# Performance work log

Hardware: AMD Instinct MI355X
Metric: run time of the kernel (lower is better)

## Reference

```python
import jax, jax.numpy as jnp
import numpy as np

B = 1024      # batch of seed nodes
S = 16        # sample_size
H = 256       # hidden
IN = 150      # in_dim + NUM_CLASS (128 + 22)
OUT = 22
HEADS = 8
NN = 100000   # number of graph nodes
LN_EPS = 1e-5


def setup_inputs() -> dict:
    key = jax.random.key(0)
    ks = jax.random.split(key, 16)
    sc = 0.05
    return {
        "node_feats": jax.random.normal(ks[0], (NN, IN), jnp.float32),
        "batch": jax.random.randint(ks[1], (B,), 0, NN),
        "nbr2": jax.random.randint(ks[2], (B, S), 0, NN),
        "nbr1": jax.random.randint(ks[3], (B * (S + 1), S), 0, NN),
        "W_in": jax.random.normal(ks[4], (IN, H), jnp.float32) * sc,
        "b_in": jnp.zeros((H,), jnp.float32),
        "Wqkv": jax.random.normal(ks[5], (2, 3, H, H), jnp.float32) * sc,
        "bqkv": jnp.zeros((2, 3, H), jnp.float32),
        "Wo": jax.random.normal(ks[6], (2, H, H), jnp.float32) * sc,
        "bo": jnp.zeros((2, H), jnp.float32),
        "Wf": jax.random.normal(ks[7], (2, H, H), jnp.float32) * sc,
        "bf": jnp.zeros((2, H), jnp.float32),
        "ln_g": jnp.ones((4, H), jnp.float32),
        "ln_b": jnp.zeros((4, H), jnp.float32),
        "W_out": jax.random.normal(ks[8], (H, OUT), jnp.float32) * sc,
        "b_out": jnp.zeros((OUT,), jnp.float32),
    }


def _layer_norm(x, g, b):
    m = jnp.mean(x, axis=-1, keepdims=True)
    v = jnp.mean((x - m) ** 2, axis=-1, keepdims=True)
    return (x - m) * jax.lax.rsqrt(v + LN_EPS) * g + b


def _mha(q, kv, Wq, Wk, Wv, bq, bk, bv, Wout, bout):
    # q: [N, 1, H], kv: [N, S, H]; single-query multi-head attention
    N, Sk, _ = kv.shape
    dh = H // HEADS
    qp = (q @ Wq + bq).reshape(N, 1, HEADS, dh)
    kp = (kv @ Wk + bk).reshape(N, Sk, HEADS, dh)
    vp = (kv @ Wv + bv).reshape(N, Sk, HEADS, dh)
    att = jax.nn.softmax(
        jnp.einsum("nqhd,nkhd->nhqk", qp, kp) / np.float32(np.sqrt(dh)), axis=-1
    )
    o = jnp.einsum("nhqk,nkhd->nqhd", att, vp).reshape(N, 1, H)
    return o @ Wout + bout


def _attn_block(x, l, Wqkv, bqkv, Wo, bo, Wf, bf, ln_g, ln_b):
    # x: [N, S+1, H]; slot 0 is the query (self), rest are sampled neighbors
    q, kv = x[:, 0:1, :], x[:, 1:, :]
    h = _mha(q, kv, Wqkv[l, 0], Wqkv[l, 1], Wqkv[l, 2],
             bqkv[l, 0], bqkv[l, 1], bqkv[l, 2], Wo[l], bo[l])
    h = h[:, 0, :] + q[:, 0, :]                       # residual
    h = _layer_norm(h, ln_g[2 * l], ln_b[2 * l])
    h = h + (h @ Wf[l] + bf[l])                       # FFN (single Linear) + residual
    return _layer_norm(h, ln_g[2 * l + 1], ln_b[2 * l + 1])


def reference(node_feats, batch, nbr2, nbr1, W_in, b_in, Wqkv, bqkv, Wo, bo,
              Wf, bf, ln_g, ln_b, W_out, b_out):
    # Recursive neighbor expansion (unrolled for layers=2)
    ids1 = jnp.concatenate([batch[:, None], nbr2], axis=1).reshape(-1)   # [B*(S+1)]
    ids0 = jnp.concatenate([ids1[:, None], nbr1], axis=1).reshape(-1)    # [B*(S+1)^2]
    # layer 0: proj_in(features) = ReLU(Linear) (Dropout identity in eval)
    h0 = jax.nn.relu(node_feats[ids0] @ W_in + b_in)                     # [M0, H]
    # layer 1
    h1 = _attn_block(h0.reshape(B * (S + 1), S + 1, H), 0,
                     Wqkv, bqkv, Wo, bo, Wf, bf, ln_g, ln_b)
    # layer 2
    h2 = _attn_block(h1.reshape(B, S + 1, H), 1,
                     Wqkv, bqkv, Wo, bo, Wf, bf, ln_g, ln_b)
    # proj_out: Linear -> Softmax
    return jax.nn.softmax(h2 @ W_out + b_out, axis=-1)
```

## Files before the change

### kernel.cpp

```cpp
#include <hip/hip_runtime.h>
#include <hip/hip_bf16.h>
#include <math.h>

typedef unsigned short ushort_t;
typedef __bf16 bf16x8 __attribute__((ext_vector_type(8)));
typedef float  f32x4  __attribute__((ext_vector_type(4)));

#define B_SZ   1024
#define SEQ    17
#define KVN    16
#define HDIM   256
#define NHEAD  8
#define DH     32
#define INF    150
#define OUTD   22
#define LN_EPS 1e-5f
#define N1     (B_SZ * SEQ)
#define NN_    100000
#define NKVBLK 1563
#define NHQBLK 272

constexpr size_t SZ_H0    = (size_t)NN_ * 256 * 2;
constexpr size_t SZ_KV0   = (size_t)NN_ * 512 * 2;
constexpr size_t SZ_ROW   = (size_t)N1 * 256 * 2;
constexpr size_t OFF_HQ   = 0;
constexpr size_t OFF_KV0  = OFF_HQ + SZ_H0;
constexpr size_t OFF_QKV1 = OFF_KV0;
constexpr size_t OFF_O1   = OFF_QKV1 + (size_t)N1 * 768 * 2;
constexpr size_t OFF_H2   = OFF_O1 + (size_t)B_SZ * 256 * 2;
constexpr size_t OFF_Q0   = OFF_KV0 + SZ_KV0;
constexpr size_t OFF_O0   = OFF_Q0 + SZ_ROW;
constexpr size_t OFF_H1   = OFF_O0;
constexpr size_t OFF_IDS  = OFF_O0 + SZ_ROW;
constexpr size_t OFF_WTIN = OFF_IDS + (size_t)N1 * 4;
constexpr size_t OFF_WKV0 = OFF_WTIN + 256 * 160 * 2;
constexpr size_t OFF_WQ0  = OFF_WKV0 + 512 * 256 * 2;
constexpr size_t OFF_WKVQ1= OFF_WQ0 + 256 * 256 * 2;
constexpr size_t OFF_WO0  = OFF_WKVQ1 + 768 * 256 * 2;
constexpr size_t OFF_WF0  = OFF_WO0 + 256 * 256 * 2;
constexpr size_t OFF_WO1  = OFF_WF0 + 256 * 256 * 2;
constexpr size_t OFF_WF1  = OFF_WO1 + 256 * 256 * 2;
constexpr size_t OFF_B1   = OFF_WF1 + 256 * 256 * 2;

__device__ __forceinline__ ushort_t f2bfu(float x) {
    __hip_bfloat16 h = __float2bfloat16(x);
    return *reinterpret_cast<ushort_t*>(&h);
}
__device__ __forceinline__ float bfu2f(ushort_t u) {
    __hip_bfloat16 h;
    *reinterpret_cast<ushort_t*>(&h) = u;
    return __bfloat162float(h);
}
__device__ __forceinline__ f32x4 mfma16(bf16x8 a, bf16x8 b, f32x4 c) {
    return __builtin_amdgcn_mfma_f32_16x16x32_bf16(a, b, c, 0, 0, 0);
}

__global__ __launch_bounds__(256) void k_prep(
    const float* __restrict__ W_in, const float* __restrict__ Wqkv,
    const float* __restrict__ Wo, const float* __restrict__ Wf,
    const float* __restrict__ bqkv,
    const int* __restrict__ batch, const int* __restrict__ nbr2,
    char* __restrict__ ws) {
    const int job = blockIdx.y;
    const int idx = blockIdx.x * 256 + threadIdx.x;
    if (job == 11) {
        if (idx < N1) {
            int b = idx / SEQ, s = idx % SEQ;
            ((int*)(ws + OFF_IDS))[idx] = (s == 0) ? batch[b] : nbr2[b * KVN + s - 1];
        }
        return;
    }
    if (job == 12) {
        if (idx < 768) ((float*)(ws + OFF_B1))[idx] = bqkv[768 + ((idx + 256) % 768)];
        return;
    }
    const float* src = nullptr; ushort_t* dst = nullptr;
    int Kpad = 256, Kvalid = 256;
    switch (job) {
        case 0:  src = W_in;           dst = (ushort_t*)(ws + OFF_WTIN); Kpad = 160; Kvalid = 150; break;
        case 1:  src = Wqkv + 65536;   dst = (ushort_t*)(ws + OFF_WKV0); break;
        case 2:  src = Wqkv + 131072;  dst = (ushort_t*)(ws + OFF_WKV0) + 65536; break;
        case 3:  src = Wqkv;           dst = (ushort_t*)(ws + OFF_WQ0); break;
        case 4:  src = Wqkv + 262144;  dst = (ushort_t*)(ws + OFF_WKVQ1); break;
        case 5:  src = Wqkv + 327680;  dst = (ushort_t*)(ws + OFF_WKVQ1) + 65536; break;
        case 6:  src = Wqkv + 196608;  dst = (ushort_t*)(ws + OFF_WKVQ1) + 131072; break;
        case 7:  src = Wo;             dst = (ushort_t*)(ws + OFF_WO0); break;
        case 8:  src = Wo + 65536;     dst = (ushort_t*)(ws + OFF_WO1); break;
        case 9:  src = Wf;             dst = (ushort_t*)(ws + OFF_WF0); break;
        case 10: src = Wf + 65536;     dst = (ushort_t*)(ws + OFF_WF1); break;
    }
    const int total = 256 * Kpad;
    if (idx >= total) return;
    int n = idx / Kpad, k = idx % Kpad;
    dst[idx] = (k < Kvalid) ? f2bfu(src[(size_t)k * 256 + n]) : (ushort_t)0;
}

__global__ __launch_bounds__(256) void k_fused(
    const float* __restrict__ nf,
    const ushort_t* __restrict__ Wt_in, const float* __restrict__ b_in,
    const ushort_t* __restrict__ Wkv, const ushort_t* __restrict__ Wq,
    const float* __restrict__ bqkv, const int* __restrict__ ids1,
    ushort_t* __restrict__ kv0, ushort_t* __restrict__ hq,
    ushort_t* __restrict__ q0) {
    __shared__ ushort_t Ah[64 * 256];
    __shared__ ushort_t Sh[4][32][72];
    const int tid = threadIdx.x;
    const bool iskv = blockIdx.x < NKVBLK;
    const int m0 = (iskv ? blockIdx.x : blockIdx.x - NKVBLK) * 64;
    const int lane = tid & 63, w = tid >> 6;
    const int lr = lane & 15, q4 = lane >> 4, lk = q4 * 8;

    {
        ushort_t (*Astage)[168] = reinterpret_cast<ushort_t (*)[168]>(Ah);
        #pragma unroll
        for (int i = 0; i < 5; ++i) {
            int flat = tid + i * 256;
            int row = flat / 20, ch = flat % 20;
            int gm; bool valid;
            if (iskv) { gm = m0 + row; valid = gm < NN_; if (!valid) gm = 0; }
            else      { gm = ids1[m0 + row]; valid = true; }
            const float* ap = nf + (size_t)gm * INF + ch * 8;
            ushort_t tmp[8];
            if (valid && ch < 18) {
                #pragma unroll
                for (int j = 0; j < 4; ++j) {
                    float2 f = *reinterpret_cast<const float2*>(ap + j * 2);
                    tmp[j * 2] = f2bfu(f.x); tmp[j * 2 + 1] = f2bfu(f.y);
                }
            } else {
                #pragma unroll
                for (int j = 0; j < 8; ++j) {
                    int k = ch * 8 + j;
                    tmp[j] = (valid && k < INF) ? f2bfu(ap[j]) : (ushort_t)0;
                }
            }
            *reinterpret_cast<int4*>(&Astage[row][ch * 8]) = *reinterpret_cast<int4*>(tmp);
        }
    }
    __syncthreads();

    f32x4 acc[4][4] = {};
    {
        ushort_t (*Astage)[168] = reinterpret_cast<ushort_t (*)[168]>(Ah);
        bf16x8 bc[4];
        #pragma unroll
        for (int ni = 0; ni < 4; ++ni)
            bc[ni] = *reinterpret_cast<const bf16x8*>(
                Wt_in + (size_t)(w * 64 + ni * 16 + lr) * 160 + lk);
        #pragma unroll
        for (int s = 0; s < 5; ++s) {
            bf16x8 bn[4];
            if (s < 4) {
                #pragma unroll
                for (int ni = 0; ni < 4; ++ni)
                    bn[ni] = *reinterpret_cast<const bf16x8*>(
                        Wt_in + (size_t)(w * 64 + ni * 16 + lr) * 160 + (s + 1) * 32 + lk);
            }
            bf16x8 a[4];
            #pragma unroll
            for (int mi = 0; mi < 4; ++mi)
                a[mi] = *reinterpret_cast<const bf16x8*>(&Astage[mi * 16 + lr][s * 32 + lk]);
            #pragma unroll
            for (int mi = 0; mi < 4; ++mi)
                #pragma unroll
                for (int ni = 0; ni < 4; ++ni)
                    acc[mi][ni] = mfma16(a[mi], bc[ni], acc[mi][ni]);
            if (s < 4) {
                #pragma unroll
                for (int ni = 0; ni < 4; ++ni) bc[ni] = bn[ni];
            }
        }
    }
    __syncthreads();

    #pragma unroll
    for (int ni = 0; ni < 4; ++ni) {
        int col = w * 64 + ni * 16 + lr;
        float bb = b_in[col];
        #pragma unroll
        for (int mi = 0; mi < 4; ++mi)
            #pragma unroll
            for (int r = 0; r < 4; ++r) {
                int row = mi * 16 + q4 * 4 + r;
                Ah[row * 256 + (col ^ ((row & 7) << 3))] =
                    f2bfu(fmaxf(acc[mi][ni][r] + bb, 0.f));
            }
    }
    __syncthreads();

    if (!iskv) {
        #pragma unroll
        for (int i = 0; i < 8; ++i) {
            int flat = tid + i * 256;
            int row = flat >> 5, ch = flat & 31;
            *reinterpret_cast<int4*>(hq + (size_t)(m0 + row) * 256 + ch * 8) =
                *reinterpret_cast<const int4*>(&Ah[row * 256 + (ch ^ (row & 7)) * 8]);
        }
    }

    const int nh = iskv ? 2 : 1;
    for (int h = 0; h < nh; ++h) {
        const ushort_t* Bm = iskv ? (Wkv + (size_t)h * 256 * 256) : Wq;
        const float* bias = iskv ? (bqkv + 256 + h * 256) : bqkv;
        f32x4 acc2[4][4] = {};
        bf16x8 bc[4];
        #pragma unroll
        for (int ni = 0; ni < 4; ++ni)
            bc[ni] = *reinterpret_cast<const bf16x8*>(
                Bm + (size_t)(w * 64 + ni * 16 + lr) * 256 + lk);
        #pragma unroll
        for (int s = 0; s < 8; ++s) {
            bf16x8 bn[4];
            if (s < 7) {
                #pragma unroll
                for (int ni = 0; ni < 4; ++ni)
                    bn[ni] = *reinterpret_cast<const bf16x8*>(
                        Bm + (size_t)(w * 64 + ni * 16 + lr) * 256 + (s + 1) * 32 + lk);
            }
            bf16x8 a[4];
            #pragma unroll
            for (int mi = 0; mi < 4; ++mi) {
                int row = mi * 16 + lr;
                int chunk = (s * 4 + q4) ^ (row & 7);
                a[mi] = *reinterpret_cast<const bf16x8*>(&Ah[row * 256 + chunk * 8]);
            }
            #pragma unroll
            for (int mi = 0; mi < 4; ++mi)
                #pragma unroll
                for (int ni = 0; ni < 4; ++ni)
                    acc2[mi][ni] = mfma16(a[mi], bc[ni], acc2[mi][ni]);
            if (s < 7) {
                #pragma unroll
                for (int ni = 0; ni < 4; ++ni) bc[ni] = bn[ni];
            }
        }
        float bl[4];
        #pragma unroll
        for (int ni = 0; ni < 4; ++ni) bl[ni] = bias[w * 64 + ni * 16 + lr];
        ushort_t* outp = iskv ? kv0 : q0;
        const int ldo = iskv ? 512 : 256;
        const int coff = (iskv ? h * 256 : 0) + w * 64;
        #pragma unroll
        for (int part = 0; part < 2; ++part) {
            #pragma unroll
            for (int mi2 = 0; mi2 < 2; ++mi2) {
                int mi = part * 2 + mi2;
                #pragma unroll
                for (int ni = 0; ni < 4; ++ni)
                    #pragma unroll
                    for (int r = 0; r < 4; ++r)
                        Sh[w][mi2 * 16 + q4 * 4 + r][ni * 16 + lr] =
                            f2bfu(acc2[mi][ni][r] + bl[ni]);
            }
            #pragma unroll
            for (int j = 0; j < 4; ++j) {
                int flat = lane + j * 64;
                int r32 = flat >> 3, ch = flat & 7;
                int grow = m0 + part * 32 + r32;
                if (!iskv || grow < NN_)
                    *reinterpret_cast<int4*>(outp + (size_t)grow * ldo + coff + ch * 8) =
                        *reinterpret_cast<const int4*>(&Sh[w][r32][ch * 8]);
            }
        }
    }
}

__global__ __launch_bounds__(256) void k_ffn(
    const ushort_t* __restrict__ Ain, const ushort_t* __restrict__ W1t,
    const float* __restrict__ b1,
    const ushort_t* __restrict__ resmat, int rstride,
    const float* __restrict__ lng1, const float* __restrict__ lnb1,
    const ushort_t* __restrict__ W2t, const float* __restrict__ b2,
    const float* __restrict__ lng2, const float* __restrict__ lnb2,
    ushort_t* __restrict__ out) {
    __shared__ ushort_t Al[32][264];
    __shared__ float xr[32][260];
    __shared__ float mrow[32], rrow[32];
    const int tid = threadIdx.x;
    const int m0 = blockIdx.x * 32;
    const int lane = tid & 63, w = tid >> 6;
    const int lr = lane & 15, q4 = lane >> 4, lk = q4 * 8;

    #pragma unroll
    for (int j = 0; j < 4; ++j) {
        int flat = tid + j * 256;
        int row = flat >> 5, ch = flat & 31;
        *reinterpret_cast<int4*>(&Al[row][ch * 8]) =
            *reinterpret_cast<const int4*>(Ain + (size_t)(m0 + row) * 256 + ch * 8);
    }
    __syncthreads();

    f32x4 acc[2][4];
    #pragma unroll
    for (int g = 0; g < 2; ++g) {
        const ushort_t* Wt = g ? W2t : W1t;
        #pragma unroll
        for (int mi = 0; mi < 2; ++mi)
            #pragma unroll
            for (int ni = 0; ni < 4; ++ni) acc[mi][ni] = f32x4{0.f, 0.f, 0.f, 0.f};
        bf16x8 bc[4];
        #pragma unroll
        for (int ni = 0; ni < 4; ++ni)
            bc[ni] = *reinterpret_cast<const bf16x8*>(
                Wt + (size_t)(w * 64 + ni * 16 + lr) * 256 + lk);
        #pragma unroll
        for (int s = 0; s < 8; ++s) {
            bf16x8 bn[4];
            if (s < 7) {
                #pragma unroll
                for (int ni = 0; ni < 4; ++ni)
                    bn[ni] = *reinterpret_cast<const bf16x8*>(
                        Wt + (size_t)(w * 64 + ni * 16 + lr) * 256 + (s + 1) * 32 + lk);
            }
            bf16x8 a0 = *reinterpret_cast<const bf16x8*>(&Al[lr][s * 32 + lk]);
            bf16x8 a1 = *reinterpret_cast<const bf16x8*>(&Al[16 + lr][s * 32 + lk]);
            #pragma unroll
            for (int ni = 0; ni < 4; ++ni) {
                acc[0][ni] = mfma16(a0, bc[ni], acc[0][ni]);
                acc[1][ni] = mfma16(a1, bc[ni], acc[1][ni]);
            }
            if (s < 7) {
                #pragma unroll
                for (int ni = 0; ni < 4; ++ni) bc[ni] = bn[ni];
            }
        }
        #pragma unroll
        for (int mi = 0; mi < 2; ++mi)
            #pragma unroll
            for (int ni = 0; ni < 4; ++ni)
                #pragma unroll
                for (int r = 0; r < 4; ++r)
                    xr[mi * 16 + q4 * 4 + r][w * 64 + ni * 16 + lr] = acc[mi][ni][r];
        __syncthreads();
        {
            float bb = g ? b2[tid] : b1[tid];
            if (g == 0) {
                for (int r = 0; r < 32; ++r)
                    xr[r][tid] += bb + bfu2f(resmat[(size_t)(m0 + r) * rstride * 256 + tid]);
            } else {
                for (int r = 0; r < 32; ++r)
                    xr[r][tid] += bb + bfu2f(Al[r][tid]);
            }
        }
        __syncthreads();
        for (int rr = w * 8; rr < w * 8 + 8; ++rr) {
            float4 v = *reinterpret_cast<const float4*>(&xr[rr][lane * 4]);
            float s1 = v.x + v.y + v.z + v.w;
            float s2 = v.x * v.x + v.y * v.y + v.z * v.z + v.w * v.w;
            #pragma unroll
            for (int off = 32; off > 0; off >>= 1) {
                s1 += __shfl_xor(s1, off);
                s2 += __shfl_xor(s2, off);
            }
            if (lane == 0) {
                float m = s1 * (1.f / 256.f);
                float var = s2 * (1.f / 256.f) - m * m;
                mrow[rr] = m;
                rrow[rr] = rsqrtf(var + LN_EPS);
            }
        }
        __syncthreads();
        if (g == 0) {
            float gg = lng1[tid], bb = lnb1[tid];
            for (int r = 0; r < 32; ++r)
                Al[r][tid] = f2bfu((xr[r][tid] - mrow[r]) * rrow[r] * gg + bb);
        } else {
            float gg = lng2[tid], bb = lnb2[tid];
            for (int r = 0; r < 32; ++r)
                out[(size_t)(m0 + r) * 256 + tid] =
                    f2bfu((xr[r][tid] - mrow[r]) * rrow[r] * gg + bb);
        }
        __syncthreads();
    }
}

__global__ __launch_bounds__(256) void k_qkv1(
    const ushort_t* __restrict__ h1, const ushort_t* __restrict__ Wt,
    const float* __restrict__ bias, ushort_t* __restrict__ outm) {
    __shared__ ushort_t Ah[64 * 256];
    __shared__ ushort_t Sh[4][32][72];
    const int tid = threadIdx.x;
    const int m0 = blockIdx.x * 64;
    const int lane = tid & 63, w = tid >> 6;
    const int lr = lane & 15, q4 = lane >> 4, lk = q4 * 8;

    #pragma unroll
    for (int i = 0; i < 8; ++i) {
        int flat = tid + i * 256;
        int row = flat >> 5, ch = flat & 31;
        *reinterpret_cast<int4*>(&Ah[row * 256 + ((ch ^ (row & 7)) * 8)]) =
            *reinterpret_cast<const int4*>(h1 + (size_t)(m0 + row) * 256 + ch * 8);
    }
    __syncthreads();

    for (int p = 0; p < 3; ++p) {
        f32x4 acc[4][4] = {};
        bf16x8 bc[4];
        #pragma unroll
        for (int ni = 0; ni < 4; ++ni)
            bc[ni] = *reinterpret_cast<const bf16x8*>(
                Wt + (size_t)(p * 256 + w * 64 + ni * 16 + lr) * 256 + lk);
        #pragma unroll
        for (int s = 0; s < 8; ++s) {
            bf16x8 bn[4];
            if (s < 7) {
                #pragma unroll
                for (int ni = 0; ni < 4; ++ni)
                    bn[ni] = *reinterpret_cast<const bf16x8*>(
                        Wt + (size_t)(p * 256 + w * 64 + ni * 16 + lr) * 256 + (s + 1) * 32 + lk);
            }
            bf16x8 a[4];
            #pragma unroll
            for (int mi = 0; mi < 4; ++mi) {
                int row = mi * 16 + lr;
                int chunk = (s * 4 + q4) ^ (row & 7);
                a[mi] = *reinterpret_cast<const bf16x8*>(&Ah[row * 256 + chunk * 8]);
            }
            #pragma unroll
            for (int mi = 0; mi < 4; ++mi)
                #pragma unroll
                for (int ni = 0; ni < 4; ++ni)
                    acc[mi][ni] = mfma16(a[mi], bc[ni], acc[mi][ni]);
            if (s < 7) {
                #pragma unroll
                for (int ni = 0; ni < 4; ++ni) bc[ni] = bn[ni];
            }
        }
        float bl[4];
        #pragma unroll
        for (int ni = 0; ni < 4; ++ni) bl[ni] = bias[p * 256 + w * 64 + ni * 16 + lr];
        const int coff = p * 256 + w * 64;
        #pragma unroll
        for (int part = 0; part < 2; ++part) {
            #pragma unroll
            for (int mi2 = 0; mi2 < 2; ++mi2) {
                int mi = part * 2 + mi2;
                #pragma unroll
                for (int ni = 0; ni < 4; ++ni)
                    #pragma unroll
                    for (int r = 0; r < 4; ++r)
                        Sh[w][mi2 * 16 + q4 * 4 + r][ni * 16 + lr] =
                            f2bfu(acc[mi][ni][r] + bl[ni]);
            }
            #pragma unroll
            for (int j = 0; j < 4; ++j) {
                int flat = lane + j * 64;
                int r32 = flat >> 3, ch = flat & 7;
                int grow = m0 + part * 32 + r32;
                *reinterpret_cast<int4*>(outm + (size_t)grow * 768 + coff + ch * 8) =
                    *reinterpret_cast<const int4*>(&Sh[w][r32][ch * 8]);
            }
        }
    }
}

__global__ __launch_bounds__(256) void attn_wave(
    const ushort_t* __restrict__ q_all, int qld, int qoff, int qstride,
    const ushort_t* __restrict__ kv_all, int kvld, int koff, int voff,
    const int* __restrict__ kvidx, int ngroups, ushort_t* __restrict__ o_out) {
    __shared__ ushort_t KL[4][KVN][264];
    __shared__ ushort_t VL[4][KVN][264];
    const int w = threadIdx.x >> 6, lane = threadIdx.x & 63;
    const int g = blockIdx.x * 4 + w;
    if (g >= ngroups) return;

    int idx16 = 0;
    if (lane < KVN)
        idx16 = kvidx ? kvidx[g * KVN + lane] : g * SEQ + 1 + lane;

    float qv[4];
    {
        uint2 u = *reinterpret_cast<const uint2*>(
            q_all + (size_t)g * qstride * qld + qoff + lane * 4);
        qv[0] = bfu2f((ushort_t)(u.x & 0xffff));
        qv[1] = bfu2f((ushort_t)(u.x >> 16));
        qv[2] = bfu2f((ushort_t)(u.y & 0xffff));
        qv[3] = bfu2f((ushort_t)(u.y >> 16));
    }
    {
        const int r = lane & 15, qtr = lane >> 4;
        int rid = __shfl(idx16, r);
        const ushort_t* kb = kv_all + (size_t)rid * kvld + koff;
        const ushort_t* vb = kv_all + (size_t)rid * kvld + voff;
        #pragma unroll
        for (int j = 0; j < 8; ++j) {
            int c8 = (qtr * 8 + j) * 8;
            *reinterpret_cast<int4*>(&KL[w][r][c8]) = *reinterpret_cast<const int4*>(kb + c8);
            *reinterpret_cast<int4*>(&VL[w][r][c8]) = *reinterpret_cast<const int4*>(vb + c8);
        }
    }
    float att[KVN];
    #pragma unroll
    for (int k = 0; k < KVN; ++k) {
        uint2 u = *reinterpret_cast<const uint2*>(&KL[w][k][lane * 4]);
        float p = qv[0] * bfu2f((ushort_t)(u.x & 0xffff))
                + qv[1] * bfu2f((ushort_t)(u.x >> 16))
                + qv[2] * bfu2f((ushort_t)(u.y & 0xffff))
                + qv[3] * bfu2f((ushort_t)(u.y >> 16));
        p += __shfl_xor(p, 1);
        p += __shfl_xor(p, 2);
        p += __shfl_xor(p, 4);
        att[k] = p * 0.17677669529663687f;
    }
    float m = att[0];
    #pragma unroll
    for (int k = 1; k < KVN; ++k) m = fmaxf(m, att[k]);
    float sum = 0.f;
    #pragma unroll
    for (int k = 0; k < KVN; ++k) { att[k] = __expf(att[k] - m); sum += att[k]; }
    float inv = 1.f / sum;
    float o[4] = {0.f, 0.f, 0.f, 0.f};
    #pragma unroll
    for (int k = 0; k < KVN; ++k) {
        uint2 u = *reinterpret_cast<const uint2*>(&VL[w][k][lane * 4]);
        float a = att[k] * inv;
        o[0] += a * bfu2f((ushort_t)(u.x & 0xffff));
        o[1] += a * bfu2f((ushort_t)(u.x >> 16));
        o[2] += a * bfu2f((ushort_t)(u.y & 0xffff));
        o[3] += a * bfu2f((ushort_t)(u.y >> 16));
    }
    uint2 r;
    r.x = (unsigned)f2bfu(o[0]) | ((unsigned)f2bfu(o[1]) << 16);
    r.y = (unsigned)f2bfu(o[2]) | ((unsigned)f2bfu(o[3]) << 16);
    *reinterpret_cast<uint2*>(o_out + (size_t)g * 256 + lane * 4) = r;
}

__global__ __launch_bounds__(64) void k_out(
    const ushort_t* __restrict__ h2, const float* __restrict__ W_out,
    const float* __restrict__ b_out, float* __restrict__ out) {
    const int b = blockIdx.x, j = threadIdx.x;
    __shared__ float xr[HDIM];
    for (int k = j; k < HDIM; k += 64) xr[k] = bfu2f(h2[(size_t)b * HDIM + k]);
    __syncthreads();
    float logit = -1e30f;
    if (j < OUTD) {
        float acc = b_out[j];
        for (int k = 0; k < HDIM; ++k) acc += xr[k] * W_out[k * OUTD + j];
        logit = acc;
    }
    float m = logit;
    #pragma unroll
    for (int off = 32; off > 0; off >>= 1) m = fmaxf(m, __shfl_xor(m, off));
    float e = (j < OUTD) ? __expf(logit - m) : 0.f;
    float s = e;
    #pragma unroll
    for (int off = 32; off > 0; off >>= 1) s += __shfl_xor(s, off);
    if (j < OUTD) out[(size_t)b * OUTD + j] = e / s;
}

extern "C" void kernel_launch(void* const* d_in, const int* in_sizes, int n_in,
                              void* d_out, int out_size, void* d_ws, size_t ws_size,
                              hipStream_t stream) {
    const float* nf    = (const float*)d_in[0];
    const int*   batch = (const int*)d_in[1];
    const int*   nbr2  = (const int*)d_in[2];
    const int*   nbr1  = (const int*)d_in[3];
    const float* W_in  = (const float*)d_in[4];
    const float* b_in  = (const float*)d_in[5];
    const float* Wqkv  = (const float*)d_in[6];
    const float* bqkv  = (const float*)d_in[7];
    const float* Wo    = (const float*)d_in[8];
    const float* bo    = (const float*)d_in[9];
    const float* Wf    = (const float*)d_in[10];
    const float* bf    = (const float*)d_in[11];
    const float* ln_g  = (const float*)d_in[12];
    const float* ln_b  = (const float*)d_in[13];
    const float* W_out = (const float*)d_in[14];
    const float* b_out = (const float*)d_in[15];
    float* out = (float*)d_out;
    char* ws = (char*)d_ws;

    ushort_t* hq   = (ushort_t*)(ws + OFF_HQ);
    ushort_t* kv0  = (ushort_t*)(ws + OFF_KV0);
    ushort_t* q0   = (ushort_t*)(ws + OFF_Q0);
    ushort_t* o0   = (ushort_t*)(ws + OFF_O0);
    ushort_t* h1   = (ushort_t*)(ws + OFF_H1);
    ushort_t* qkv1 = (ushort_t*)(ws + OFF_QKV1);
    ushort_t* o1   = (ushort_t*)(ws + OFF_O1);
    ushort_t* h2   = (ushort_t*)(ws + OFF_H2);
    const int* ids1 = (const int*)(ws + OFF_IDS);

    hipLaunchKernelGGL(k_prep, dim3(256, 13), dim3(256), 0, stream,
                       W_in, Wqkv, Wo, Wf, bqkv, batch, nbr2, ws);
    hipLaunchKernelGGL(k_fused, dim3(NKVBLK + NHQBLK), dim3(256), 0, stream,
                       nf, (const ushort_t*)(ws + OFF_WTIN), b_in,
                       (const ushort_t*)(ws + OFF_WKV0),
                       (const ushort_t*)(ws + OFF_WQ0), bqkv, ids1,
                       kv0, hq, q0);
    hipLaunchKernelGGL(attn_wave, dim3(N1 / 4), dim3(256), 0, stream,
                       q0, 256, 0, 1, kv0, 512, 0, 256, nbr1, N1, o0);
    hipLaunchKernelGGL(k_ffn, dim3(N1 / 32), dim3(256), 0, stream,
                       o0, (const ushort_t*)(ws + OFF_WO0), bo,
                       hq, 1, ln_g, ln_b,
                       (const ushort_t*)(ws + OFF_WF0), bf,
                       ln_g + 256, ln_b + 256, h1);
    hipLaunchKernelGGL(k_qkv1, dim3(N1 / 64), dim3(256), 0, stream,
                       h1, (const ushort_t*)(ws + OFF_WKVQ1),
                       (const float*)(ws + OFF_B1), qkv1);
    hipLaunchKernelGGL(attn_wave, dim3(B_SZ / 4), dim3(256), 0, stream,
                       qkv1, 768, 512, 17, qkv1, 768, 0, 256,
                       (const int*)nullptr, B_SZ, o1);
    hipLaunchKernelGGL(k_ffn, dim3(B_SZ / 32), dim3(256), 0, stream,
                       o1, (const ushort_t*)(ws + OFF_WO1), bo + 256,
                       h1, 17, ln_g + 512, ln_b + 512,
                       (const ushort_t*)(ws + OFF_WF1), bf + 256,
                       ln_g + 768, ln_b + 768, h2);
    hipLaunchKernelGGL(k_out, dim3(B_SZ), dim3(64), 0, stream,
                       h2, W_out, b_out, out);
}
```

Baseline: 288.4 us.

## Stage weight tiles into LDS via async global_load_lds double buffering

The fused projection kernel now streams B-matrix (weight) K-slices into a double-buffered, XOR-swizzled LDS buffer with global_load_lds, where before each wave loaded weight fragments directly from global memory into registers. The aim is to cut redundant per-wave global reads and let the loads overlap the MFMA work. The price is a __syncthreads per K-step, a larger LDS footprint (the output staging area now reuses the B buffer), and removal of the validity masking for out-of-range rows in the A staging. That last change loads row 0 features in place of zeros; those rows are not stored, so the result stays correct.

```diff
diff --git a/kernel.cpp b/kernel.cpp
--- a/kernel.cpp
+++ b/kernel.cpp
@@ -5,6 +5,8 @@
 typedef unsigned short ushort_t;
 typedef __bf16 bf16x8 __attribute__((ext_vector_type(8)));
 typedef float  f32x4  __attribute__((ext_vector_type(4)));
+typedef __attribute__((address_space(1))) const unsigned int* gas_t;
+typedef __attribute__((address_space(3))) unsigned int* las_t;
 
 #define B_SZ   1024
 #define SEQ    17
@@ -55,6 +57,21 @@
     return __builtin_amdgcn_mfma_f32_16x16x32_bf16(a, b, c, 0, 0, 0);
 }
 
+__device__ __forceinline__ void stage_b(
+    const ushort_t* __restrict__ Bsrc, int Kld, int kk,
+    ushort_t* lbase, int w, int lane) {
+    #pragma unroll
+    for (int i = 0; i < 4; ++i) {
+        int inst = w * 4 + i;
+        int row = inst * 16 + (lane >> 2);
+        int q_log = (lane & 3) ^ ((row >> 1) & 3);
+        const ushort_t* src = Bsrc + (size_t)row * Kld + kk + q_log * 8;
+        __builtin_amdgcn_global_load_lds((gas_t)(const void*)src,
+                                         (las_t)(void*)(lbase + inst * 512),
+                                         16, 0, 0);
+    }
+}
+
 __global__ __launch_bounds__(256) void k_prep(
     const float* __restrict__ W_in, const float* __restrict__ Wqkv,
     const float* __restrict__ Wo, const float* __restrict__ Wf,
@@ -103,7 +120,7 @@
     ushort_t* __restrict__ kv0, ushort_t* __restrict__ hq,
     ushort_t* __restrict__ q0) {
     __shared__ ushort_t Ah[64 * 256];
-    __shared__ ushort_t Sh[4][32][72];
+    __shared__ ushort_t Bbuf[2 * 8192];
     const int tid = threadIdx.x;
     const bool iskv = blockIdx.x < NKVBLK;
     const int m0 = (iskv ? blockIdx.x : blockIdx.x - NKVBLK) * 64;
@@ -116,12 +133,12 @@
         for (int i = 0; i < 5; ++i) {
             int flat = tid + i * 256;
             int row = flat / 20, ch = flat % 20;
-            int gm; bool valid;
-            if (iskv) { gm = m0 + row; valid = gm < NN_; if (!valid) gm = 0; }
-            else      { gm = ids1[m0 + row]; valid = true; }
+            int gm; 
+            if (iskv) { gm = m0 + row; if (gm >= NN_) gm = 0; }
+            else      { gm = ids1[m0 + row]; }
             const float* ap = nf + (size_t)gm * INF + ch * 8;
             ushort_t tmp[8];
-            if (valid && ch < 18) {
+            if (ch < 18) {
                 #pragma unroll
                 for (int j = 0; j < 4; ++j) {
                     float2 f = *reinterpret_cast<const float2*>(ap + j * 2);
@@ -131,47 +148,39 @@
                 #pragma unroll
                 for (int j = 0; j < 8; ++j) {
                     int k = ch * 8 + j;
-                    tmp[j] = (valid && k < INF) ? f2bfu(ap[j]) : (ushort_t)0;
+                    tmp[j] = (k < INF) ? f2bfu(ap[j]) : (ushort_t)0;
                 }
             }
             *reinterpret_cast<int4*>(&Astage[row][ch * 8]) = *reinterpret_cast<int4*>(tmp);
         }
     }
+    stage_b(Wt_in, 160, 0, Bbuf, w, lane);
     __syncthreads();
 
-    f32x4 acc[4][4] = {};
+    f32x4 acc1[4][4] = {};
     {
         ushort_t (*Astage)[168] = reinterpret_cast<ushort_t (*)[168]>(Ah);
-        bf16x8 bc[4];
-        #pragma unroll
-        for (int ni = 0; ni < 4; ++ni)
-            bc[ni] = *reinterpret_cast<const bf16x8*>(
-                Wt_in + (size_t)(w * 64 + ni * 16 + lr) * 160 + lk);
-        #pragma unroll
         for (int s = 0; s < 5; ++s) {
-            bf16x8 bn[4];
-            if (s < 4) {
-                #pragma unroll
-                for (int ni = 0; ni < 4; ++ni)
-                    bn[ni] = *reinterpret_cast<const bf16x8*>(
-                        Wt_in + (size_t)(w * 64 + ni * 16 + lr) * 160 + (s + 1) * 32 + lk);
-            }
-            bf16x8 a[4];
+            const int cur = s & 1;
+            if (s < 4) stage_b(Wt_in, 160, (s + 1) * 32, Bbuf + (cur ^ 1) * 8192, w, lane);
+            bf16x8 a[4], b[4];
             #pragma unroll
             for (int mi = 0; mi < 4; ++mi)
                 a[mi] = *reinterpret_cast<const bf16x8*>(&Astage[mi * 16 + lr][s * 32 + lk]);
             #pragma unroll
+            for (int ni = 0; ni < 4; ++ni) {
+                int n = w * 64 + ni * 16 + lr;
+                b[ni] = *reinterpret_cast<const bf16x8*>(
+                    &Bbuf[cur * 8192 + n * 32 + ((q4 ^ ((n >> 1) & 3)) * 8)]);
+            }
+            #pragma unroll
             for (int mi = 0; mi < 4; ++mi)
                 #pragma unroll
                 for (int ni = 0; ni < 4; ++ni)
-                    acc[mi][ni] = mfma16(a[mi], bc[ni], acc[mi][ni]);
-            if (s < 4) {
-                #pragma unroll
-                for (int ni = 0; ni < 4; ++ni) bc[ni] = bn[ni];
-            }
-        }
-    }
-    __syncthreads();
+                    acc1[mi][ni] = mfma16(a[mi], b[ni], acc1[mi][ni]);
+            __syncthreads();
+        }
+    }
 
     #pragma unroll
     for (int ni = 0; ni < 4; ++ni) {
@@ -183,7 +192,7 @@
             for (int r = 0; r < 4; ++r) {
                 int row = mi * 16 + q4 * 4 + r;
                 Ah[row * 256 + (col ^ ((row & 7) << 3))] =
-                    f2bfu(fmaxf(acc[mi][ni][r] + bb, 0.f));
+                    f2bfu(fmaxf(acc1[mi][ni][r] + bb, 0.f));
             }
     }
     __syncthreads();
@@ -194,30 +203,22 @@
             int flat = tid + i * 256;
             int row = flat >> 5, ch = flat & 31;
             *reinterpret_cast<int4*>(hq + (size_t)(m0 + row) * 256 + ch * 8) =
-                *reinterpret_cast<const int4*>(&Ah[row * 256 + (ch ^ (row & 7)) * 8]);
-        }
-    }
-
-    const int nh = iskv ? 2 : 1;
-    for (int h = 0; h < nh; ++h) {
-        const ushort_t* Bm = iskv ? (Wkv + (size_t)h * 256 * 256) : Wq;
+                *reinterpret_cast<const int4*>(&Ah[row * 256 + ((ch ^ (row & 7)) * 8)]);
+        }
+    }
+
+    const int npass = iskv ? 2 : 1;
+    for (int h = 0; h < npass; ++h) {
+        const ushort_t* Bm = iskv ? (Wkv + (size_t)h * 65536) : Wq;
         const float* bias = iskv ? (bqkv + 256 + h * 256) : bqkv;
+        __syncthreads();
+        stage_b(Bm, 256, 0, Bbuf, w, lane);
+        __syncthreads();
         f32x4 acc2[4][4] = {};
-        bf16x8 bc[4];
-        #pragma unroll
-        for (int ni = 0; ni < 4; ++ni)
-            bc[ni] = *reinterpret_cast<const bf16x8*>(
-                Bm + (size_t)(w * 64 + ni * 16 + lr) * 256 + lk);
-        #pragma unroll
         for (int s = 0; s < 8; ++s) {
-            bf16x8 bn[4];
-            if (s < 7) {
-                #pragma unroll
-                for (int ni = 0; ni < 4; ++ni)
-                    bn[ni] = *reinterpret_cast<const bf16x8*>(
-                        Bm + (size_t)(w * 64 + ni * 16 + lr) * 256 + (s + 1) * 32 + lk);
-            }
-            bf16x8 a[4];
+            const int cur = s & 1;
+            if (s < 7) stage_b(Bm, 256, (s + 1) * 32, Bbuf + (cur ^ 1) * 8192, w, lane);
+            bf16x8 a[4], b[4];
             #pragma unroll
             for (int mi = 0; mi < 4; ++mi) {
                 int row = mi * 16 + lr;
@@ -225,14 +226,17 @@
                 a[mi] = *reinterpret_cast<const bf16x8*>(&Ah[row * 256 + chunk * 8]);
             }
             #pragma unroll
+            for (int ni = 0; ni < 4; ++ni) {
+                int n = w * 64 + ni * 16 + lr;
+                b[ni] = *reinterpret_cast<const bf16x8*>(
+                    &Bbuf[cur * 8192 + n * 32 + ((q4 ^ ((n >> 1) & 3)) * 8)]);
+            }
+            #pragma unroll
             for (int mi = 0; mi < 4; ++mi)
                 #pragma unroll
                 for (int ni = 0; ni < 4; ++ni)
-                    acc2[mi][ni] = mfma16(a[mi], bc[ni], acc2[mi][ni]);
-            if (s < 7) {
-                #pragma unroll
-                for (int ni = 0; ni < 4; ++ni) bc[ni] = bn[ni];
-            }
+                    acc2[mi][ni] = mfma16(a[mi], b[ni], acc2[mi][ni]);
+            __syncthreads();
         }
         float bl[4];
         #pragma unroll
@@ -240,6 +244,7 @@
         ushort_t* outp = iskv ? kv0 : q0;
         const int ldo = iskv ? 512 : 256;
         const int coff = (iskv ? h * 256 : 0) + w * 64;
+        ushort_t* Shw = Bbuf + w * 32 * 72;
         #pragma unroll
         for (int part = 0; part < 2; ++part) {
             #pragma unroll
@@ -249,7 +254,7 @@
                 for (int ni = 0; ni < 4; ++ni)
                     #pragma unroll
                     for (int r = 0; r < 4; ++r)
-                        Sh[w][mi2 * 16 + q4 * 4 + r][ni * 16 + lr] =
+                        Shw[(mi2 * 16 + q4 * 4 + r) * 72 + ni * 16 + lr] =
                             f2bfu(acc2[mi][ni][r] + bl[ni]);
             }
             #pragma unroll
@@ -259,7 +264,7 @@
                 int grow = m0 + part * 32 + r32;
                 if (!iskv || grow < NN_)
                     *reinterpret_cast<int4*>(outp + (size_t)grow * ldo + coff + ch * 8) =
-                        *reinterpret_cast<const int4*>(&Sh[w][r32][ch * 8]);
+                        *reinterpret_cast<const int4*>(&Shw[r32 * 72 + ch * 8]);
             }
         }
     }
```

After: 275.8 us. 4.4% less time.
